# Performance work log

Measured on AMD Instinct MI355X. Metric: run time of the kernel, lower is better.

Reference implementation:

```python
import jax, jax.numpy as jnp
import numpy as np

B, T, F = 512, 256, 64
H = [128, 256, 128, 64]

def _glorot(key, shape):
    fan_in, fan_out = shape[0], shape[1]
    lim = np.sqrt(6.0 / (fan_in + fan_out))
    return jax.random.uniform(key, shape, jnp.float32, -lim, lim)

def setup_inputs() -> dict:
    key = jax.random.key(0)
    ks = jax.random.split(key, 16)
    inp = {"x": jax.random.normal(ks[0], (B, T, F), jnp.float32)}
    dims = [F] + H
    for i in range(4):
        inp[f"Wx{i+1}"] = _glorot(ks[1 + 3 * i], (dims[i], dims[i + 1]))
        # keras uses orthogonal recurrent init; scaled normal is an acceptable stand-in
        q, _ = jnp.linalg.qr(jax.random.normal(ks[2 + 3 * i], (dims[i + 1], dims[i + 1])))
        inp[f"Wh{i+1}"] = q.astype(jnp.float32)
        inp[f"b{i+1}"] = jnp.zeros((dims[i + 1],), jnp.float32)
    inp["Wd"] = _glorot(ks[13], (T * H[-1], 1))
    inp["bd"] = jnp.zeros((1,), jnp.float32)
    return inp

def simple_rnn(x, Wx, Wh, b):
    # x: [B, T, Fin] -> hidden sequence [B, T, H]; h_t = relu(x_t Wx + h_{t-1} Wh + b)
    xp = jnp.einsum('btf,fh->tbh', x, Wx) + b  # precompute input projection, time-major
    h0 = jnp.zeros((x.shape[0], Wh.shape[0]), x.dtype)
    def step(h, xt):
        h = jax.nn.relu(xt + h @ Wh)
        return h, h
    _, hs = jax.lax.scan(step, h0, xp)  # hs: [T, B, H]
    return jnp.transpose(hs, (1, 0, 2))

def reference(x, Wx1, Wh1, b1, Wx2, Wh2, b2, Wx3, Wh3, b3, Wx4, Wh4, b4, Wd, bd):
    h = simple_rnn(x, Wx1, Wh1, b1)   # dropout layers are identity at inference
    h = simple_rnn(h, Wx2, Wh2, b2)
    h = simple_rnn(h, Wx3, Wh3, b3)
    h = simple_rnn(h, Wx4, Wh4, b4)
    flat = h.reshape(h.shape[0], -1)  # [B, T*64]
    return flat @ Wd + bd             # [B, 1]
```

## Files before the change

### kernel.cpp

```cpp
#include <hip/hip_runtime.h>
#include <hip/hip_bf16.h>

#define BB 512
#define TT 256

typedef __attribute__((ext_vector_type(8))) short bf16x8;
typedef __attribute__((ext_vector_type(4))) float f32x4;

__device__ __forceinline__ unsigned short f2b(float f) {
    union { float f; unsigned u; } v; v.f = f;
    unsigned r = v.u + 0x7FFFu + ((v.u >> 16) & 1u);
    return (unsigned short)(r >> 16);
}
__device__ __forceinline__ float b2f(unsigned short h) {
    union { unsigned u; float f; } v; v.u = ((unsigned)h) << 16;
    return v.f;
}
__device__ __forceinline__ ushort2 pk2(float a, float b) {
    __hip_bfloat162 h = __float22bfloat162_rn(float2{a, b});
    union { __hip_bfloat162 h; ushort2 u; } v; v.h = h; return v.u;
}


__global__ __launch_bounds__(256) void cvt_tile4(const float* __restrict__ x,
                                                 unsigned short* __restrict__ xb) {
    const int s = blockIdx.x >> 6;
    const int tg = blockIdx.x & 63;
    const int tid = threadIdx.x;
    const int b = (tid >> 1) & 15;
    const int f0 = (tid >> 5) * 8 + (tid & 1) * 4;
    const float* xrow = &x[(((size_t)(s * 16 + b) * TT) + tg * 4) * 64 + f0];
    unsigned short* ob = &xb[((size_t)(s * TT) + tg * 4) * 1024 + tid * 4];
#pragma unroll
    for (int tt = 0; tt < 4; ++tt) {
        float4 v = *reinterpret_cast<const float4*>(xrow + tt * 64);
        ushort2 lo = pk2(v.x, v.y), hi = pk2(v.z, v.w);
        ushort4 o; o.x = lo.x; o.y = lo.y; o.z = hi.x; o.w = hi.y;
        *reinterpret_cast<ushort4*>(ob + tt * 1024) = o;
    }
}

__global__ __launch_bounds__(512) __attribute__((amdgpu_waves_per_eu(2, 2))) void rnn4(
    const unsigned short* __restrict__ Xb,
    const float* __restrict__ Wx1, const float* __restrict__ Wh1, const float* __restrict__ b1,
    const float* __restrict__ Wx2, const float* __restrict__ Wh2, const float* __restrict__ b2,
    const float* __restrict__ Wx3, const float* __restrict__ Wh3, const float* __restrict__ b3,
    const float* __restrict__ Wx4, const float* __restrict__ Wh4, const float* __restrict__ b4,
    unsigned short* __restrict__ H4) {
    const int tid = threadIdx.x;
    const int s = blockIdx.x;
    const int w = tid >> 6;
    const int lane = tid & 63;
    const int l15 = lane & 15;
    const int quad = lane >> 4;
    const int rdo = quad * 128 + l15 * 8;

    __shared__ __align__(16) unsigned short hall[2][9216];

    bf16x8 wreg[48];
    f32x4 bvv[6];

#define LOADW(BASE, WP, H_, CB, KC_, MT_)                                          \
    _Pragma("unroll")                                                              \
    for (int mt = 0; mt < MT_; ++mt) {                                             \
        int m = (CB) + mt * 16 + l15;                                              \
        _Pragma("unroll")                                                          \
        for (int kc = 0; kc < KC_; ++kc)                                           \
            _Pragma("unroll")                                                      \
            for (int j = 0; j < 8; ++j)                                            \
                wreg[(BASE) + kc * MT_ + mt][j] =                                  \
                    (short)f2b(WP[(kc * 32 + quad * 8 + j) * H_ + m]);             \
    }
#define LOADBF(OFF, BP, CB, MT_)                                                   \
    _Pragma("unroll")                                                              \
    for (int mt = 0; mt < MT_; ++mt) {                                             \
        float4 t4v = *reinterpret_cast<const float4*>((BP) + (CB) + mt * 16 + quad * 4); \
        bvv[(OFF) + mt][0] = t4v.x; bvv[(OFF) + mt][1] = t4v.y;                    \
        bvv[(OFF) + mt][2] = t4v.z; bvv[(OFF) + mt][3] = t4v.w;                    \
    }

    if (w < 2) {
        LOADW(0,  Wh1, 128, w * 64, 4, 4)
        LOADW(16, Wx1, 128, w * 64, 2, 4)
        LOADW(24, Wh4, 64,  w * 32, 2, 2)
        LOADW(28, Wx4, 64,  w * 32, 4, 2)
        LOADBF(0, b1, w * 64, 4)
        LOADBF(4, b4, w * 32, 2)
    } else if (w < 6) {
        __builtin_amdgcn_s_setprio(1);
        LOADW(0,  Wh2, 256, (w - 2) * 64, 8, 4)
        LOADW(32, Wx2, 256, (w - 2) * 64, 4, 4)
        LOADBF(0, b2, (w - 2) * 64, 4)
    } else {
        LOADW(0,  Wh3, 128, (w - 6) * 64, 4, 4)
        LOADW(16, Wx3, 128, (w - 6) * 64, 8, 4)
        LOADBF(0, b3, (w - 6) * 64, 4)
    }
#undef LOADW
#undef LOADBF

    for (int i = tid; i < 2 * 9216; i += 512) (&hall[0][0])[i] = 0;

    const unsigned short* Xs = Xb + (size_t)s * TT * 1024;
    unsigned short* H4s = H4 + (size_t)s * TT * 1024;

    if (w < 2) {
#pragma unroll
        for (int kx = 0; kx < 2; ++kx) {
            wreg[36 + kx] = *reinterpret_cast<const bf16x8*>(&Xs[kx * 512 + rdo]);
            wreg[38 + kx] = *reinterpret_cast<const bf16x8*>(&Xs[1024 + kx * 512 + rdo]);
        }
    }
    __syncthreads();

    const unsigned short* xp0 = Xs + 2 * 1024 + rdo;
    const unsigned short* xp1 = Xs + 3 * 1024 + rdo;

    const int wro1 = (w * 8 + (quad >> 1)) * 128 + l15 * 8 + (quad & 1) * 4;
    const int wro4 = 8192 + (w * 4 + (quad >> 1)) * 128 + l15 * 8 + (quad & 1) * 4;
    const int wro2 = 2048 + ((w - 2) * 8 + (quad >> 1)) * 128 + l15 * 8 + (quad & 1) * 4;
    const int wro3 = 6144 + ((w - 6) * 8 + (quad >> 1)) * 128 + l15 * 8 + (quad & 1) * 4;

    unsigned short* op_e = H4s + 1024 + (wro4 - 8192);
    unsigned short* op_o = H4s + (wro4 - 8192);

#define PACKMK(ACC_MT)                                                             \
    ushort2 lo = pk2(fmaxf((ACC_MT)[0], 0.f), fmaxf((ACC_MT)[1], 0.f));            \
    ushort2 hi = pk2(fmaxf((ACC_MT)[2], 0.f), fmaxf((ACC_MT)[3], 0.f));            \
    ushort4 o; o.x = lo.x; o.y = lo.y; o.z = hi.x; o.w = hi.y;

#define STEP(TAU_, RP_, WP_, XAB, XPP, OPP)                                        \
    {                                                                              \
        const int tau_ = (TAU_);                                                   \
        const unsigned short* RB = &hall[RP_][0];                                  \
        unsigned short* WB = &hall[WP_][0];                                        \
        if (w < 2) {                                                               \
            if ((unsigned)tau_ < TT) {                                     \
                f32x4 acc[4];                                                      \
                _Pragma("unroll")                                                  \
                for (int mt = 0; mt < 4; ++mt)                                     \
                    acc[mt] = __builtin_amdgcn_mfma_f32_16x16x32_bf16(             \
                        wreg[16 + mt], wreg[(XAB) + 0], bvv[mt], 0, 0, 0);         \
                _Pragma("unroll")                                                  \
                for (int mt = 0; mt < 4; ++mt)                                     \
                    acc[mt] = __builtin_amdgcn_mfma_f32_16x16x32_bf16(             \
                        wreg[20 + mt], wreg[(XAB) + 1], acc[mt], 0, 0, 0);         \
                if (tau_ + 2 < TT) {                                               \
                    wreg[(XAB) + 0] = *reinterpret_cast<const bf16x8*>(XPP);       \
                    wreg[(XAB) + 1] = *reinterpret_cast<const bf16x8*>(XPP + 512); \
                    XPP += 2048;                                                   \
                }                                                                  \
                _Pragma("unroll")                                                  \
                for (int kc = 0; kc < 4; ++kc) {                                   \
                    bf16x8 af = *reinterpret_cast<const bf16x8*>(&RB[rdo + kc * 512]); \
                    _Pragma("unroll")                                              \
                    for (int mt = 0; mt < 4; ++mt)                                 \
                        acc[mt] = __builtin_amdgcn_mfma_f32_16x16x32_bf16(         \
                            wreg[kc * 4 + mt], af, acc[mt], 0, 0, 0);              \
                }                                                                  \
                _Pragma("unroll")                                                  \
                for (int mt = 0; mt < 4; ++mt) {                                   \
                    PACKMK(acc[mt])                                                \
                    *reinterpret_cast<ushort4*>(&WB[wro1 + mt * 256]) = o;         \
                }                                                                  \
            }                                                                      \
            if ((unsigned)(tau_ - 3) < TT) {                               \
                f32x4 acc[2];                                                      \
                {                                                                  \
                    bf16x8 af0 = *reinterpret_cast<const bf16x8*>(&RB[6144 + rdo]); \
                    _Pragma("unroll")                                              \
                    for (int mt = 0; mt < 2; ++mt)                                 \
                        acc[mt] = __builtin_amdgcn_mfma_f32_16x16x32_bf16(         \
                            wreg[28 + mt], af0, bvv[4 + mt], 0, 0, 0);             \
                }                                                                  \
                _Pragma("unroll")                                                  \
                for (int kx = 1; kx < 4; ++kx) {                                   \
                    bf16x8 af = *reinterpret_cast<const bf16x8*>(&RB[6144 + rdo + kx * 512]); \
                    _Pragma("unroll")                                              \
                    for (int mt = 0; mt < 2; ++mt)                                 \
                        acc[mt] = __builtin_amdgcn_mfma_f32_16x16x32_bf16(         \
                            wreg[28 + kx * 2 + mt], af, acc[mt], 0, 0, 0);         \
                }                                                                  \
                _Pragma("unroll")                                                  \
                for (int kc = 0; kc < 2; ++kc) {                                   \
                    bf16x8 af = *reinterpret_cast<const bf16x8*>(&RB[8192 + rdo + kc * 512]); \
                    _Pragma("unroll")                                              \
                    for (int mt = 0; mt < 2; ++mt)                                 \
                        acc[mt] = __builtin_amdgcn_mfma_f32_16x16x32_bf16(         \
                            wreg[24 + kc * 2 + mt], af, acc[mt], 0, 0, 0);         \
                }                                                                  \
                _Pragma("unroll")                                                  \
                for (int mt = 0; mt < 2; ++mt) {                                   \
                    PACKMK(acc[mt])                                                \
                    *reinterpret_cast<ushort4*>(&WB[wro4 + mt * 256]) = o;         \
                    *reinterpret_cast<ushort4*>(OPP + mt * 256) = o;               \
                }                                                                  \
                OPP += 2048;                                                       \
            }                                                                      \
        } else if (w < 6) {                                                        \
            if ((unsigned)(tau_ - 1) < TT) {                               \
                f32x4 acc[4];                                                      \
                {                                                                  \
                    bf16x8 af0 = *reinterpret_cast<const bf16x8*>(&RB[rdo]);       \
                    _Pragma("unroll")                                              \
                    for (int mt = 0; mt < 4; ++mt)                                 \
                        acc[mt] = __builtin_amdgcn_mfma_f32_16x16x32_bf16(         \
                            wreg[32 + mt], af0, bvv[mt], 0, 0, 0);                 \
                }                                                                  \
                _Pragma("unroll")                                                  \
                for (int kx = 1; kx < 4; ++kx) {                                   \
                    bf16x8 af = *reinterpret_cast<const bf16x8*>(&RB[rdo + kx * 512]); \
                    _Pragma("unroll")                                              \
                    for (int mt = 0; mt < 4; ++mt)                                 \
                        acc[mt] = __builtin_amdgcn_mfma_f32_16x16x32_bf16(         \
                            wreg[32 + kx * 4 + mt], af, acc[mt], 0, 0, 0);         \
                }                                                                  \
                _Pragma("unroll")                                                  \
                for (int kc = 0; kc < 8; ++kc) {                                   \
                    bf16x8 af = *reinterpret_cast<const bf16x8*>(&RB[2048 + rdo + kc * 512]); \
                    _Pragma("unroll")                                              \
                    for (int mt = 0; mt < 4; ++mt)                                 \
                        acc[mt] = __builtin_amdgcn_mfma_f32_16x16x32_bf16(         \
                            wreg[kc * 4 + mt], af, acc[mt], 0, 0, 0);              \
                }                                                                  \
                _Pragma("unroll")                                                  \
                for (int mt = 0; mt < 4; ++mt) {                                   \
                    PACKMK(acc[mt])                                                \
                    *reinterpret_cast<ushort4*>(&WB[wro2 + mt * 256]) = o;         \
                }                                                                  \
            }                                                                      \
        } else {                                                                   \
            if ((unsigned)(tau_ - 2) < TT) {                               \
                f32x4 acc[4];                                                      \
                {                                                                  \
                    bf16x8 af0 = *reinterpret_cast<const bf16x8*>(&RB[2048 + rdo]); \
                    _Pragma("unroll")                                              \
                    for (int mt = 0; mt < 4; ++mt)                                 \
                        acc[mt] = __builtin_amdgcn_mfma_f32_16x16x32_bf16(         \
                            wreg[16 + mt], af0, bvv[mt], 0, 0, 0);                 \
                }                                                                  \
                _Pragma("unroll")                                                  \
                for (int kx = 1; kx < 8; ++kx) {                                   \
                    bf16x8 af = *reinterpret_cast<const bf16x8*>(&RB[2048 + rdo + kx * 512]); \
                    _Pragma("unroll")                                              \
                    for (int mt = 0; mt < 4; ++mt)                                 \
                        acc[mt] = __builtin_amdgcn_mfma_f32_16x16x32_bf16(         \
                            wreg[16 + kx * 4 + mt], af, acc[mt], 0, 0, 0);         \
                }                                                                  \
                _Pragma("unroll")                                                  \
                for (int kc = 0; kc < 4; ++kc) {                                   \
                    bf16x8 af = *reinterpret_cast<const bf16x8*>(&RB[6144 + rdo + kc * 512]); \
                    _Pragma("unroll")                                              \
                    for (int mt = 0; mt < 4; ++mt)                                 \
                        acc[mt] = __builtin_amdgcn_mfma_f32_16x16x32_bf16(         \
                            wreg[kc * 4 + mt], af, acc[mt], 0, 0, 0);              \
                }                                                                  \
                _Pragma("unroll")                                                  \
                for (int mt = 0; mt < 4; ++mt) {                                   \
                    PACKMK(acc[mt])                                                \
                    *reinterpret_cast<ushort4*>(&WB[wro3 + mt * 256]) = o;         \
                }                                                                  \
            }                                                                      \
        }                                                                          \
        __builtin_amdgcn_s_waitcnt(0xC07F);                                        \
        __builtin_amdgcn_s_barrier();                                              \
    }

#pragma unroll 1
    for (int tau = 0; tau < TT + 3; tau += 2) {
        STEP(tau, 0, 1, 36, xp0, op_e)
        STEP(tau + 1, 1, 0, 38, xp1, op_o)
    }
#undef STEP
#undef PACKMK
}

__global__ __launch_bounds__(256) void dense_part(const unsigned short* __restrict__ Ht,
                                                  const float* __restrict__ Wd,
                                                  float* __restrict__ part) {
    __shared__ float red[16][17];
    const int s = blockIdx.x >> 3;
    const int tc = blockIdx.x & 7;
    const int tid = threadIdx.x;
    const int b = (tid >> 1) & 15;
    const int kbase = (tid >> 5) * 8 + (tid & 1) * 4;
    const unsigned short* base = Ht + ((size_t)s * TT + tc * 32) * 1024 + tid * 4;
    float acc = 0.f;
    for (int t = 0; t < 32; ++t) {
        ushort4 v = *reinterpret_cast<const ushort4*>(base + (size_t)t * 1024);
        const float* wd = &Wd[(tc * 32 + t) * 64 + kbase];
        acc += b2f(v.x) * wd[0] + b2f(v.y) * wd[1] + b2f(v.z) * wd[2] + b2f(v.w) * wd[3];
    }
    red[b][(tid >> 5) * 2 + (tid & 1)] = acc;
    __syncthreads();
    if (tid < 16) {
        float sum = 0.f;
#pragma unroll
        for (int j = 0; j < 16; ++j) sum += red[tid][j];
        part[blockIdx.x * 16 + tid] = sum;
    }
}

__global__ __launch_bounds__(512) void dense_final(const float* __restrict__ part,
                                                   const float* __restrict__ bd,
                                                   float* __restrict__ out) {
    const int i = threadIdx.x;
    const int s = i >> 4, b = i & 15;
    float sum = bd[0];
#pragma unroll
    for (int tc = 0; tc < 8; ++tc) sum += part[(s * 8 + tc) * 16 + b];
    out[i] = sum;
}

extern "C" void kernel_launch(void* const* d_in, const int* in_sizes, int n_in,
                              void* d_out, int out_size, void* d_ws, size_t ws_size,
                              hipStream_t stream) {
    (void)in_sizes; (void)n_in; (void)out_size; (void)ws_size;
    const float* x   = (const float*)d_in[0];
    const float* Wx1 = (const float*)d_in[1];
    const float* Wh1 = (const float*)d_in[2];
    const float* b1  = (const float*)d_in[3];
    const float* Wx2 = (const float*)d_in[4];
    const float* Wh2 = (const float*)d_in[5];
    const float* b2  = (const float*)d_in[6];
    const float* Wx3 = (const float*)d_in[7];
    const float* Wh3 = (const float*)d_in[8];
    const float* b3  = (const float*)d_in[9];
    const float* Wx4 = (const float*)d_in[10];
    const float* Wh4 = (const float*)d_in[11];
    const float* b4  = (const float*)d_in[12];
    const float* Wd  = (const float*)d_in[13];
    const float* bd  = (const float*)d_in[14];
    float* out = (float*)d_out;

    char* ws = (char*)d_ws;
    unsigned short* xbT  = (unsigned short*)(ws);
    unsigned short* H4   = (unsigned short*)(ws + 16777216);
    float*          part = (float*)(ws + 2 * 16777216);

    cvt_tile4<<<2048, 256, 0, stream>>>(x, xbT);

    rnn4<<<32, 512, 0, stream>>>(xbT, Wx1, Wh1, b1, Wx2, Wh2, b2,
                                 Wx3, Wh3, b3, Wx4, Wh4, b4, H4);

    dense_part<<<256, 256, 0, stream>>>(H4, Wd, part);
    dense_final<<<1, 512, 0, stream>>>(part, bd, out);
}
```

Measured before the change: 424.5 us.

## Precompute layer-1 input projection in parallel kernel and fuse dense head into RNN

The layer-1 input projection x·Wx1 moves out of the serial recurrent loop into a separate, fully parallel MFMA kernel that writes bf16 preactivations. The recurrent kernel now only adds those values to the bias, which removes eight MFMAs per step from the critical path for waves 0-1. The final dense layer is also folded into the recurrent kernel: each step multiplies the layer-4 outputs by Wd, accumulates per thread, and reduces through shared memory at the end. This drops the H4 global writes and two extra launches, at the cost of rounding the projection to bf16 before the bias is added and a larger intermediate buffer (2048 per timestep instead of 1024).

```diff
diff --git a/kernel.cpp b/kernel.cpp
--- a/kernel.cpp
+++ b/kernel.cpp
@@ -1,7 +1,6 @@
 #include <hip/hip_runtime.h>
 #include <hip/hip_bf16.h>
 
-#define BB 512
 #define TT 256
 
 typedef __attribute__((ext_vector_type(8))) short bf16x8;
@@ -22,31 +21,65 @@
 }
 
 
-__global__ __launch_bounds__(256) void cvt_tile4(const float* __restrict__ x,
-                                                 unsigned short* __restrict__ xb) {
-    const int s = blockIdx.x >> 6;
-    const int tg = blockIdx.x & 63;
-    const int tid = threadIdx.x;
-    const int b = (tid >> 1) & 15;
-    const int f0 = (tid >> 5) * 8 + (tid & 1) * 4;
-    const float* xrow = &x[(((size_t)(s * 16 + b) * TT) + tg * 4) * 64 + f0];
-    unsigned short* ob = &xb[((size_t)(s * TT) + tg * 4) * 1024 + tid * 4];
-#pragma unroll
-    for (int tt = 0; tt < 4; ++tt) {
-        float4 v = *reinterpret_cast<const float4*>(xrow + tt * 64);
-        ushort2 lo = pk2(v.x, v.y), hi = pk2(v.z, v.w);
-        ushort4 o; o.x = lo.x; o.y = lo.y; o.z = hi.x; o.w = hi.y;
-        *reinterpret_cast<ushort4*>(ob + tt * 1024) = o;
+__global__ __launch_bounds__(256) void xw1(const float* __restrict__ x,
+                                           const float* __restrict__ Wx1,
+                                           unsigned short* __restrict__ a1) {
+    const int s = blockIdx.x >> 3;
+    const int tg = blockIdx.x & 7;
+    const int wv = threadIdx.x >> 6;
+    const int lane = threadIdx.x & 63;
+    const int l15 = lane & 15;
+    const int quad = lane >> 4;
+    const int t0 = tg * 32 + wv * 8;
+
+    bf16x8 wf[16];
+#pragma unroll
+    for (int kc = 0; kc < 2; ++kc)
+#pragma unroll
+        for (int mt = 0; mt < 8; ++mt)
+#pragma unroll
+            for (int j = 0; j < 8; ++j)
+                wf[kc * 8 + mt][j] =
+                    (short)f2b(Wx1[(kc * 32 + quad * 8 + j) * 128 + mt * 16 + l15]);
+
+    const float* xr = x + ((size_t)(s * 16 + l15) * TT + t0) * 64 + quad * 8;
+    unsigned short* ob = a1 + ((size_t)s * TT + t0) * 2048 + (quad * 16 + l15) * 16;
+
+#pragma unroll 2
+    for (int i = 0; i < 8; ++i) {
+        bf16x8 xf[2];
+#pragma unroll
+        for (int kx = 0; kx < 2; ++kx) {
+            float4 va = *reinterpret_cast<const float4*>(xr + i * 64 + kx * 32);
+            float4 vb = *reinterpret_cast<const float4*>(xr + i * 64 + kx * 32 + 4);
+            ushort2 p0 = pk2(va.x, va.y), p1 = pk2(va.z, va.w);
+            ushort2 p2 = pk2(vb.x, vb.y), p3 = pk2(vb.z, vb.w);
+            bf16x8 r;
+            r[0] = p0.x; r[1] = p0.y; r[2] = p1.x; r[3] = p1.y;
+            r[4] = p2.x; r[5] = p2.y; r[6] = p3.x; r[7] = p3.y;
+            xf[kx] = r;
+        }
+#pragma unroll
+        for (int mt = 0; mt < 8; ++mt) {
+            f32x4 z = {0.f, 0.f, 0.f, 0.f};
+            f32x4 acc = __builtin_amdgcn_mfma_f32_16x16x32_bf16(wf[mt], xf[0], z, 0, 0, 0);
+            acc = __builtin_amdgcn_mfma_f32_16x16x32_bf16(wf[8 + mt], xf[1], acc, 0, 0, 0);
+            ushort2 lo = pk2(acc[0], acc[1]), hi = pk2(acc[2], acc[3]);
+            ushort4 o; o.x = lo.x; o.y = lo.y; o.z = hi.x; o.w = hi.y;
+            *reinterpret_cast<ushort4*>(ob + (size_t)i * 2048 + (mt >> 2) * 1024 +
+                                        (mt & 3) * 4) = o;
+        }
     }
 }
 
 __global__ __launch_bounds__(512) __attribute__((amdgpu_waves_per_eu(2, 2))) void rnn4(
-    const unsigned short* __restrict__ Xb,
-    const float* __restrict__ Wx1, const float* __restrict__ Wh1, const float* __restrict__ b1,
+    const unsigned short* __restrict__ A1,
+    const float* __restrict__ Wh1, const float* __restrict__ b1,
     const float* __restrict__ Wx2, const float* __restrict__ Wh2, const float* __restrict__ b2,
     const float* __restrict__ Wx3, const float* __restrict__ Wh3, const float* __restrict__ b3,
     const float* __restrict__ Wx4, const float* __restrict__ Wh4, const float* __restrict__ b4,
-    unsigned short* __restrict__ H4) {
+    const float* __restrict__ Wd, const float* __restrict__ bd,
+    float* __restrict__ out) {
     const int tid = threadIdx.x;
     const int s = blockIdx.x;
     const int w = tid >> 6;
@@ -81,7 +114,6 @@
 
     if (w < 2) {
         LOADW(0,  Wh1, 128, w * 64, 4, 4)
-        LOADW(16, Wx1, 128, w * 64, 2, 4)
         LOADW(24, Wh4, 64,  w * 32, 2, 2)
         LOADW(28, Wx4, 64,  w * 32, 4, 2)
         LOADBF(0, b1, w * 64, 4)
@@ -101,54 +133,58 @@
 
     for (int i = tid; i < 2 * 9216; i += 512) (&hall[0][0])[i] = 0;
 
-    const unsigned short* Xs = Xb + (size_t)s * TT * 1024;
-    unsigned short* H4s = H4 + (size_t)s * TT * 1024;
-
+    bf16x8 aE[2], aO[2];
+    float dacc = 0.f;
+    const unsigned short* Ab =
+        A1 + (size_t)s * TT * 2048 + (size_t)w * 1024 + (size_t)(quad * 16 + l15) * 16;
     if (w < 2) {
-#pragma unroll
-        for (int kx = 0; kx < 2; ++kx) {
-            wreg[36 + kx] = *reinterpret_cast<const bf16x8*>(&Xs[kx * 512 + rdo]);
-            wreg[38 + kx] = *reinterpret_cast<const bf16x8*>(&Xs[1024 + kx * 512 + rdo]);
-        }
+        aE[0] = *reinterpret_cast<const bf16x8*>(Ab);
+        aE[1] = *reinterpret_cast<const bf16x8*>(Ab + 8);
+        aO[0] = *reinterpret_cast<const bf16x8*>(Ab + 2048);
+        aO[1] = *reinterpret_cast<const bf16x8*>(Ab + 2048 + 8);
     }
     __syncthreads();
 
-    const unsigned short* xp0 = Xs + 2 * 1024 + rdo;
-    const unsigned short* xp1 = Xs + 3 * 1024 + rdo;
+    const unsigned short* aq0 = Ab + 2 * 2048;
+    const unsigned short* aq1 = Ab + 3 * 2048;
 
     const int wro1 = (w * 8 + (quad >> 1)) * 128 + l15 * 8 + (quad & 1) * 4;
     const int wro4 = 8192 + (w * 4 + (quad >> 1)) * 128 + l15 * 8 + (quad & 1) * 4;
     const int wro2 = 2048 + ((w - 2) * 8 + (quad >> 1)) * 128 + l15 * 8 + (quad & 1) * 4;
     const int wro3 = 6144 + ((w - 6) * 8 + (quad >> 1)) * 128 + l15 * 8 + (quad & 1) * 4;
 
-    unsigned short* op_e = H4s + 1024 + (wro4 - 8192);
-    unsigned short* op_o = H4s + (wro4 - 8192);
-
 #define PACKMK(ACC_MT)                                                             \
     ushort2 lo = pk2(fmaxf((ACC_MT)[0], 0.f), fmaxf((ACC_MT)[1], 0.f));            \
     ushort2 hi = pk2(fmaxf((ACC_MT)[2], 0.f), fmaxf((ACC_MT)[3], 0.f));            \
     ushort4 o; o.x = lo.x; o.y = lo.y; o.z = hi.x; o.w = hi.y;
 
-#define STEP(TAU_, RP_, WP_, XAB, XPP, OPP)                                        \
+#define STEP(TAU_, RP_, WP_, AREG, APP)                                            \
     {                                                                              \
         const int tau_ = (TAU_);                                                   \
         const unsigned short* RB = &hall[RP_][0];                                  \
         unsigned short* WB = &hall[WP_][0];                                        \
         if (w < 2) {                                                               \
-            if ((unsigned)tau_ < TT) {                                     \
+            const int t4_ = tau_ - 3;                                              \
+            float4 wd0 = {0.f, 0.f, 0.f, 0.f}, wd1 = {0.f, 0.f, 0.f, 0.f};         \
+            if ((unsigned)t4_ < TT) {   \
+                const float* wp_ = Wd + (size_t)t4_ * 64 + w * 32 + quad * 4;      \
+                wd0 = *reinterpret_cast<const float4*>(wp_);                       \
+                wd1 = *reinterpret_cast<const float4*>(wp_ + 16);                  \
+            }                                                                      \
+            if ((unsigned)tau_ < TT) {        \
                 f32x4 acc[4];                                                      \
                 _Pragma("unroll")                                                  \
-                for (int mt = 0; mt < 4; ++mt)                                     \
-                    acc[mt] = __builtin_amdgcn_mfma_f32_16x16x32_bf16(             \
-                        wreg[16 + mt], wreg[(XAB) + 0], bvv[mt], 0, 0, 0);         \
-                _Pragma("unroll")                                                  \
-                for (int mt = 0; mt < 4; ++mt)                                     \
-                    acc[mt] = __builtin_amdgcn_mfma_f32_16x16x32_bf16(             \
-                        wreg[20 + mt], wreg[(XAB) + 1], acc[mt], 0, 0, 0);         \
+                for (int mt = 0; mt < 4; ++mt) {                                   \
+                    acc[mt] = bvv[mt];                                             \
+                    _Pragma("unroll")                                              \
+                    for (int j = 0; j < 4; ++j)                                    \
+                        acc[mt][j] += b2f(                                         \
+                            (unsigned short)AREG[(mt * 4 + j) >> 3][(mt * 4 + j) & 7]); \
+                }                                                                  \
                 if (tau_ + 2 < TT) {                                               \
-                    wreg[(XAB) + 0] = *reinterpret_cast<const bf16x8*>(XPP);       \
-                    wreg[(XAB) + 1] = *reinterpret_cast<const bf16x8*>(XPP + 512); \
-                    XPP += 2048;                                                   \
+                    AREG[0] = *reinterpret_cast<const bf16x8*>(APP);               \
+                    AREG[1] = *reinterpret_cast<const bf16x8*>(APP + 8);           \
+                    APP += 4096;                                                   \
                 }                                                                  \
                 _Pragma("unroll")                                                  \
                 for (int kc = 0; kc < 4; ++kc) {                                   \
@@ -164,7 +200,7 @@
                     *reinterpret_cast<ushort4*>(&WB[wro1 + mt * 256]) = o;         \
                 }                                                                  \
             }                                                                      \
-            if ((unsigned)(tau_ - 3) < TT) {                               \
+            if ((unsigned)t4_ < TT) {             \
                 f32x4 acc[2];                                                      \
                 {                                                                  \
                     bf16x8 af0 = *reinterpret_cast<const bf16x8*>(&RB[6144 + rdo]); \
@@ -191,11 +227,14 @@
                 }                                                                  \
                 _Pragma("unroll")                                                  \
                 for (int mt = 0; mt < 2; ++mt) {                                   \
-                    PACKMK(acc[mt])                                                \
+                    float r0 = fmaxf(acc[mt][0], 0.f), r1 = fmaxf(acc[mt][1], 0.f); \
+                    float r2 = fmaxf(acc[mt][2], 0.f), r3 = fmaxf(acc[mt][3], 0.f); \
+                    ushort2 lo = pk2(r0, r1), hi = pk2(r2, r3);                    \
+                    ushort4 o; o.x = lo.x; o.y = lo.y; o.z = hi.x; o.w = hi.y;     \
                     *reinterpret_cast<ushort4*>(&WB[wro4 + mt * 256]) = o;         \
-                    *reinterpret_cast<ushort4*>(OPP + mt * 256) = o;               \
-                }                                                                  \
-                OPP += 2048;                                                       \
+                    const float4 wdv = mt ? wd1 : wd0;                             \
+                    dacc += r0 * wdv.x + r1 * wdv.y + r2 * wdv.z + r3 * wdv.w;     \
+                }                                                                  \
             }                                                                      \
         } else if (w < 6) {                                                        \
             if ((unsigned)(tau_ - 1) < TT) {                               \
@@ -268,48 +307,23 @@
 
 #pragma unroll 1
     for (int tau = 0; tau < TT + 3; tau += 2) {
-        STEP(tau, 0, 1, 36, xp0, op_e)
-        STEP(tau + 1, 1, 0, 38, xp1, op_o)
+        STEP(tau, 0, 1, aE, aq0)
+        STEP(tau + 1, 1, 0, aO, aq1)
     }
 #undef STEP
 #undef PACKMK
-}
-
-__global__ __launch_bounds__(256) void dense_part(const unsigned short* __restrict__ Ht,
-                                                  const float* __restrict__ Wd,
-                                                  float* __restrict__ part) {
-    __shared__ float red[16][17];
-    const int s = blockIdx.x >> 3;
-    const int tc = blockIdx.x & 7;
-    const int tid = threadIdx.x;
-    const int b = (tid >> 1) & 15;
-    const int kbase = (tid >> 5) * 8 + (tid & 1) * 4;
-    const unsigned short* base = Ht + ((size_t)s * TT + tc * 32) * 1024 + tid * 4;
-    float acc = 0.f;
-    for (int t = 0; t < 32; ++t) {
-        ushort4 v = *reinterpret_cast<const ushort4*>(base + (size_t)t * 1024);
-        const float* wd = &Wd[(tc * 32 + t) * 64 + kbase];
-        acc += b2f(v.x) * wd[0] + b2f(v.y) * wd[1] + b2f(v.z) * wd[2] + b2f(v.w) * wd[3];
-    }
-    red[b][(tid >> 5) * 2 + (tid & 1)] = acc;
-    __syncthreads();
-    if (tid < 16) {
-        float sum = 0.f;
-#pragma unroll
-        for (int j = 0; j < 16; ++j) sum += red[tid][j];
-        part[blockIdx.x * 16 + tid] = sum;
-    }
-}
-
-__global__ __launch_bounds__(512) void dense_final(const float* __restrict__ part,
-                                                   const float* __restrict__ bd,
-                                                   float* __restrict__ out) {
-    const int i = threadIdx.x;
-    const int s = i >> 4, b = i & 15;
-    float sum = bd[0];
-#pragma unroll
-    for (int tc = 0; tc < 8; ++tc) sum += part[(s * 8 + tc) * 16 + b];
-    out[i] = sum;
+
+    {
+        float* red = reinterpret_cast<float*>(&hall[0][0]);
+        if (w < 2) red[(w * 4 + quad) * 16 + l15] = dacc;
+        __syncthreads();
+        if (tid < 16) {
+            float sum = bd[0];
+#pragma unroll
+            for (int j = 0; j < 8; ++j) sum += red[j * 16 + tid];
+            out[s * 16 + tid] = sum;
+        }
+    }
 }
 
 extern "C" void kernel_launch(void* const* d_in, const int* in_sizes, int n_in,
@@ -333,16 +347,10 @@
     const float* bd  = (const float*)d_in[14];
     float* out = (float*)d_out;
 
-    char* ws = (char*)d_ws;
-    unsigned short* xbT  = (unsigned short*)(ws);
-    unsigned short* H4   = (unsigned short*)(ws + 16777216);
-    float*          part = (float*)(ws + 2 * 16777216);
-
-    cvt_tile4<<<2048, 256, 0, stream>>>(x, xbT);
-
-    rnn4<<<32, 512, 0, stream>>>(xbT, Wx1, Wh1, b1, Wx2, Wh2, b2,
-                                 Wx3, Wh3, b3, Wx4, Wh4, b4, H4);
-
-    dense_part<<<256, 256, 0, stream>>>(H4, Wd, part);
-    dense_final<<<1, 512, 0, stream>>>(part, bd, out);
-}
+    unsigned short* a1 = (unsigned short*)d_ws;
+
+    xw1<<<256, 256, 0, stream>>>(x, Wx1, a1);
+
+    rnn4<<<32, 512, 0, stream>>>(a1, Wh1, b1, Wx2, Wh2, b2,
+                                 Wx3, Wh3, b3, Wx4, Wh4, b4, Wd, bd, out);
+}
```

After: 553.3 us. +30.3%, slower.

## Fuse final dense projection into the RNN kernel and drop H4 writes

Applied to the files above, without the earlier changes.

The final dense layer moves into the recurrent kernel. Waves 0-1 read each layer-4 hidden state from shared memory a few steps later, multiply it by prefetched Wd slices and keep a per-thread running dot product, then reduce through shared memory at the end. This removes the global store of the full layer-4 sequence and two extra kernel launches. The cost is more work and registers on the layer-1/4 waves, which sit on the serial critical path of every step.

```diff
diff --git a/kernel.cpp b/kernel.cpp
--- a/kernel.cpp
+++ b/kernel.cpp
@@ -46,7 +46,8 @@
     const float* __restrict__ Wx2, const float* __restrict__ Wh2, const float* __restrict__ b2,
     const float* __restrict__ Wx3, const float* __restrict__ Wh3, const float* __restrict__ b3,
     const float* __restrict__ Wx4, const float* __restrict__ Wh4, const float* __restrict__ b4,
-    unsigned short* __restrict__ H4) {
+    const float* __restrict__ Wd, const float* __restrict__ bd,
+    float* __restrict__ out) {
     const int tid = threadIdx.x;
     const int s = blockIdx.x;
     const int w = tid >> 6;
@@ -102,39 +103,62 @@
     for (int i = tid; i < 2 * 9216; i += 512) (&hall[0][0])[i] = 0;
 
     const unsigned short* Xs = Xb + (size_t)s * TT * 1024;
-    unsigned short* H4s = H4 + (size_t)s * TT * 1024;
-
+
+    float4 wdE[2], wdO[2];
+    float dacc = 0.f;
+    const float* WdL = Wd + (w * 4 + quad) * 8;
     if (w < 2) {
 #pragma unroll
         for (int kx = 0; kx < 2; ++kx) {
             wreg[36 + kx] = *reinterpret_cast<const bf16x8*>(&Xs[kx * 512 + rdo]);
             wreg[38 + kx] = *reinterpret_cast<const bf16x8*>(&Xs[1024 + kx * 512 + rdo]);
         }
+        wdE[0] = *reinterpret_cast<const float4*>(WdL);
+        wdE[1] = *reinterpret_cast<const float4*>(WdL + 4);
+        wdO[0] = *reinterpret_cast<const float4*>(WdL + 64);
+        wdO[1] = *reinterpret_cast<const float4*>(WdL + 68);
     }
     __syncthreads();
 
     const unsigned short* xp0 = Xs + 2 * 1024 + rdo;
     const unsigned short* xp1 = Xs + 3 * 1024 + rdo;
+    const float* wdp0 = WdL + 2 * 64;
+    const float* wdp1 = WdL + 3 * 64;
 
     const int wro1 = (w * 8 + (quad >> 1)) * 128 + l15 * 8 + (quad & 1) * 4;
     const int wro4 = 8192 + (w * 4 + (quad >> 1)) * 128 + l15 * 8 + (quad & 1) * 4;
     const int wro2 = 2048 + ((w - 2) * 8 + (quad >> 1)) * 128 + l15 * 8 + (quad & 1) * 4;
     const int wro3 = 6144 + ((w - 6) * 8 + (quad >> 1)) * 128 + l15 * 8 + (quad & 1) * 4;
 
-    unsigned short* op_e = H4s + 1024 + (wro4 - 8192);
-    unsigned short* op_o = H4s + (wro4 - 8192);
-
 #define PACKMK(ACC_MT)                                                             \
     ushort2 lo = pk2(fmaxf((ACC_MT)[0], 0.f), fmaxf((ACC_MT)[1], 0.f));            \
     ushort2 hi = pk2(fmaxf((ACC_MT)[2], 0.f), fmaxf((ACC_MT)[3], 0.f));            \
     ushort4 o; o.x = lo.x; o.y = lo.y; o.z = hi.x; o.w = hi.y;
 
-#define STEP(TAU_, RP_, WP_, XAB, XPP, OPP)                                        \
+#define STEP(TAU_, RP_, WP_, XAB, XPP, WDV, WDP)                                   \
     {                                                                              \
         const int tau_ = (TAU_);                                                   \
         const unsigned short* RB = &hall[RP_][0];                                  \
         unsigned short* WB = &hall[WP_][0];                                        \
         if (w < 2) {                                                               \
+            const int td_ = tau_ - 4;                                              \
+            if ((unsigned)td_ < TT) {           \
+                bf16x8 hv = *reinterpret_cast<const bf16x8*>(                      \
+                    &RB[8192 + (w * 4 + quad) * 128 + l15 * 8]);                   \
+                dacc += b2f((unsigned short)hv[0]) * WDV[0].x +                    \
+                        b2f((unsigned short)hv[1]) * WDV[0].y +                    \
+                        b2f((unsigned short)hv[2]) * WDV[0].z +                    \
+                        b2f((unsigned short)hv[3]) * WDV[0].w +                    \
+                        b2f((unsigned short)hv[4]) * WDV[1].x +                    \
+                        b2f((unsigned short)hv[5]) * WDV[1].y +                    \
+                        b2f((unsigned short)hv[6]) * WDV[1].z +                    \
+                        b2f((unsigned short)hv[7]) * WDV[1].w;                     \
+                if (td_ + 2 < TT) {                                                \
+                    WDV[0] = *reinterpret_cast<const float4*>(WDP);                \
+                    WDV[1] = *reinterpret_cast<const float4*>(WDP + 4);            \
+                    WDP += 128;                                                    \
+                }                                                                  \
+            }                                                                      \
             if ((unsigned)tau_ < TT) {                                     \
                 f32x4 acc[4];                                                      \
                 _Pragma("unroll")                                                  \
@@ -193,9 +217,7 @@
                 for (int mt = 0; mt < 2; ++mt) {                                   \
                     PACKMK(acc[mt])                                                \
                     *reinterpret_cast<ushort4*>(&WB[wro4 + mt * 256]) = o;         \
-                    *reinterpret_cast<ushort4*>(OPP + mt * 256) = o;               \
-                }                                                                  \
-                OPP += 2048;                                                       \
+                }                                                                  \
             }                                                                      \
         } else if (w < 6) {                                                        \
             if ((unsigned)(tau_ - 1) < TT) {                               \
@@ -268,48 +290,23 @@
 
 #pragma unroll 1
     for (int tau = 0; tau < TT + 3; tau += 2) {
-        STEP(tau, 0, 1, 36, xp0, op_e)
-        STEP(tau + 1, 1, 0, 38, xp1, op_o)
+        STEP(tau, 0, 1, 36, xp0, wdE, wdp0)
+        STEP(tau + 1, 1, 0, 38, xp1, wdO, wdp1)
     }
 #undef STEP
 #undef PACKMK
-}
-
-__global__ __launch_bounds__(256) void dense_part(const unsigned short* __restrict__ Ht,
-                                                  const float* __restrict__ Wd,
-                                                  float* __restrict__ part) {
-    __shared__ float red[16][17];
-    const int s = blockIdx.x >> 3;
-    const int tc = blockIdx.x & 7;
-    const int tid = threadIdx.x;
-    const int b = (tid >> 1) & 15;
-    const int kbase = (tid >> 5) * 8 + (tid & 1) * 4;
-    const unsigned short* base = Ht + ((size_t)s * TT + tc * 32) * 1024 + tid * 4;
-    float acc = 0.f;
-    for (int t = 0; t < 32; ++t) {
-        ushort4 v = *reinterpret_cast<const ushort4*>(base + (size_t)t * 1024);
-        const float* wd = &Wd[(tc * 32 + t) * 64 + kbase];
-        acc += b2f(v.x) * wd[0] + b2f(v.y) * wd[1] + b2f(v.z) * wd[2] + b2f(v.w) * wd[3];
-    }
-    red[b][(tid >> 5) * 2 + (tid & 1)] = acc;
-    __syncthreads();
-    if (tid < 16) {
-        float sum = 0.f;
+
+    {
+        float* red = reinterpret_cast<float*>(&hall[0][0]);
+        if (w < 2) red[(w * 4 + quad) * 16 + l15] = dacc;
+        __syncthreads();
+        if (tid < 16) {
+            float sum = bd[0];
 #pragma unroll
-        for (int j = 0; j < 16; ++j) sum += red[tid][j];
-        part[blockIdx.x * 16 + tid] = sum;
-    }
-}
-
-__global__ __launch_bounds__(512) void dense_final(const float* __restrict__ part,
-                                                   const float* __restrict__ bd,
-                                                   float* __restrict__ out) {
-    const int i = threadIdx.x;
-    const int s = i >> 4, b = i & 15;
-    float sum = bd[0];
-#pragma unroll
-    for (int tc = 0; tc < 8; ++tc) sum += part[(s * 8 + tc) * 16 + b];
-    out[i] = sum;
+            for (int j = 0; j < 8; ++j) sum += red[j * 16 + tid];
+            out[s * 16 + tid] = sum;
+        }
+    }
 }
 
 extern "C" void kernel_launch(void* const* d_in, const int* in_sizes, int n_in,
@@ -333,16 +330,10 @@
     const float* bd  = (const float*)d_in[14];
     float* out = (float*)d_out;
 
-    char* ws = (char*)d_ws;
-    unsigned short* xbT  = (unsigned short*)(ws);
-    unsigned short* H4   = (unsigned short*)(ws + 16777216);
-    float*          part = (float*)(ws + 2 * 16777216);
+    unsigned short* xbT = (unsigned short*)d_ws;
 
     cvt_tile4<<<2048, 256, 0, stream>>>(x, xbT);
 
     rnn4<<<32, 512, 0, stream>>>(xbT, Wx1, Wh1, b1, Wx2, Wh2, b2,
-                                 Wx3, Wh3, b3, Wx4, Wh4, b4, H4);
-
-    dense_part<<<256, 256, 0, stream>>>(H4, Wd, part);
-    dense_final<<<1, 512, 0, stream>>>(part, bd, out);
-}
+                                 Wx3, Wh3, b3, Wx4, Wh4, b4, Wd, bd, out);
+}
```

Result: slower. 554.6 us (+30.7%).
